# Kernel optimization log

Measured on AMD Instinct MI355X. Metric: run time of the kernel, lower is better.

## Reference

```python
import jax, jax.numpy as jnp
import numpy as np

P, D, K, E, ITERS, THRESH, NCLS = 16, 384, 16, 8, 10, 0.9, 1000


def _forward(x, pw, pb, ln_g, ln_b, pos, qw, qb, kw, kb, vw, vb,
             ew, eb, nw, nb, m1w, m1b, m2w, m2b, fbw, fbb, fgw, fgb, cw, cb):
    B, C, H, W = x.shape
    Hp, Wp = H // P, W // P
    # patch embedding: conv(k=s=P) == reshape + matmul; (c, ph, pw) ordering matches conv weight layout
    xp = x.reshape(B, C, Hp, P, Wp, P).transpose(0, 2, 4, 1, 3, 5).reshape(B, Hp * Wp, C * P * P)
    patches = xp @ pw + pb                                    # [B, N, D]
    # layer norm (eps=1e-5)
    mu = patches.mean(-1, keepdims=True)
    var = patches.var(-1, keepdims=True)
    pn = (patches - mu) / jnp.sqrt(var + 1e-5) * ln_g + ln_b
    # k-means (Lloyd, fixed iters, deterministic evenly-spaced init)
    N = pn.shape[1]
    init_idx = jnp.linspace(0, N - 1, K).astype(jnp.int32)
    centers0 = pn[:, init_idx]                                # [B, K, D]
    pn_sq = jnp.sum(pn * pn, -1)                              # [B, N]

    def kstep(centers, _):
        d2 = (pn_sq[:, :, None]
              - 2.0 * jnp.einsum('bnd,bkd->bnk', pn, centers)
              + jnp.sum(centers * centers, -1)[:, None, :])   # [B, N, K]
        oh = jax.nn.one_hot(jnp.argmin(d2, -1), K, dtype=pn.dtype)
        counts = oh.sum(1)                                    # [B, K]
        new = jnp.einsum('bnk,bnd->bkd', oh, pn) / jnp.maximum(counts, 1.0)[:, :, None]
        new = jnp.where(counts[:, :, None] > 0, new, centers)
        return new, None

    clusters, _ = jax.lax.scan(kstep, centers0, None, length=ITERS)  # [B, K, D]
    # attention over clusters
    clusters = clusters + pos
    Q = clusters @ qw + qb
    Kt = clusters @ kw + kb
    V = clusters @ vw + vb
    attn = jax.nn.softmax(jnp.einsum('bqd,bkd->bqk', Q, Kt) / jnp.sqrt(jnp.float32(D)), -1)
    clusters = jnp.einsum('bqk,bkd->bqd', attn, V)
    # hypergraph laplacian
    hw = jax.nn.softmax(clusters @ ew + eb, axis=1)           # [B, K, E], softmax over nodes
    Dd = hw.sum(1)                                            # [B, E]
    Hm = hw.transpose(0, 2, 1)                                # [B, E, K]
    M = (Dd ** -0.5)[:, :, None] * Hm                         # D^{-1/2} H
    L = jnp.eye(E, dtype=clusters.dtype) - jnp.einsum('bek,bfk->bef', M, Hm)  # [B, E, E]
    L = jnp.pad(L, ((0, 0), (0, K - E), (0, K - E)))          # pad to [B, K, K]
    clusters = jnp.einsum('bij,bjd->bid', L, clusters)
    clusters = clusters @ nw + nb
    # non-linear propagation MLP (exact GELU, torch default)
    clusters = jax.nn.gelu(clusters @ m1w + m1b, approximate=False) @ m2w + m2b
    # adaptive node collapse: mask from ORIGINAL clusters, sequential in-place merges
    nrm = jnp.maximum(jnp.linalg.norm(clusters, axis=-1, keepdims=True), 1e-12)
    nc = clusters / nrm
    sim = jnp.einsum('bqd,bkd->bqk', nc, nc)
    mask_any = jnp.any(sim > THRESH, axis=0)                  # [K, K]: merge pair if ANY batch exceeds
    for i in range(K):                                        # small fixed K; matches sequential torch loop
        for j in range(i + 1, K):
            cond = mask_any[i, j]
            merged = (clusters[:, i] + clusters[:, j]) * 0.5
            clusters = clusters.at[:, i].set(jnp.where(cond, merged, clusters[:, i]))
            clusters = clusters.at[:, j].set(jnp.where(cond, merged, clusters[:, j]))
    # feedback modulation
    g = clusters.mean(1)                                      # [B, D]
    fb = g @ fbw + fbb
    gate = jax.nn.sigmoid(g @ fgw + fgb)                      # [B, 1]
    clusters = clusters + fb[:, None, :] * gate[:, None, :]
    return clusters.reshape(B, -1) @ cw + cb                  # [B, num_classes]


def setup_inputs() -> dict:
    key = jax.random.key(0)
    ks = jax.random.split(key, 16)
    Wm = lambda k, *s: jax.random.normal(k, s, jnp.float32) * 0.02
    z = lambda *s: jnp.zeros(s, jnp.float32)
    return {
        'x': jax.random.normal(ks[0], (128, 3, 224, 224), jnp.float32),
        'pw': Wm(ks[1], 3 * P * P, D), 'pb': z(D),
        'ln_g': jnp.ones((D,), jnp.float32), 'ln_b': z(D),
        'pos': Wm(ks[2], K, D),
        'qw': Wm(ks[3], D, D), 'qb': z(D),
        'kw': Wm(ks[4], D, D), 'kb': z(D),
        'vw': Wm(ks[5], D, D), 'vb': z(D),
        'ew': Wm(ks[6], D, E), 'eb': z(E),
        'nw': Wm(ks[7], D, D), 'nb': z(D),
        'm1w': Wm(ks[8], D, D), 'm1b': z(D),
        'm2w': Wm(ks[9], D, D), 'm2b': z(D),
        'fbw': Wm(ks[10], D, D), 'fbb': z(D),
        'fgw': Wm(ks[11], D, 1), 'fgb': z(1),
        'cw': Wm(ks[12], D * K, NCLS), 'cb': z(NCLS),
    }


def reference(x, pw, pb, ln_g, ln_b, pos, qw, qb, kw, kb, vw, vb,
              ew, eb, nw, nb, m1w, m1b, m2w, m2b, fbw, fbb, fgw, fgb, cw, cb):
    return _forward(x, pw, pb, ln_g, ln_b, pos, qw, qb, kw, kb, vw, vb,
                    ew, eb, nw, nb, m1w, m1b, m2w, m2b, fbw, fbb, fgw, fgb, cw, cb)
```

## Files before the change

kernel.cpp:

```cpp
#include <hip/hip_runtime.h>
#include <math.h>

#define NBATCH 128
#define NPTS   196
#define DIN    768
#define DM     384
#define KCL    16
#define NEXP   8
#define NITER  10
#define NCLS   1000

__global__ __launch_bounds__(256) void init_kernel(const float* __restrict__ cb,
                                                   float* __restrict__ out,
                                                   int* __restrict__ mask) {
    int idx = blockIdx.x * 256 + threadIdx.x;
    if (idx < NBATCH * NCLS) {
        out[idx] = cb[idx % NCLS];
    } else if (idx < NBATCH * NCLS + 256) {
        mask[idx - NBATCH * NCLS] = 0;
    }
}

#define BKP 16
__global__ __launch_bounds__(512, 4) void patch_ln_kernel(
        const float* __restrict__ x, const float* __restrict__ pw,
        const float* __restrict__ pb, const float* __restrict__ lng,
        const float* __restrict__ lnb, float* __restrict__ pn,
        float* __restrict__ pnsq) {
    __shared__ float As[BKP * 68];
    __shared__ float Ws[BKP * DM];
    const int tid = threadIdx.x;
    const int m0  = blockIdx.x * 64;
    const int rg  = tid >> 6;
    const int cg  = tid & 63;
    const int lr = (tid & 255) >> 2, kq = tid & 3;
    const int m  = m0 + lr;
    const int bi = m / NPTS, n = m - bi * NPTS;
    const int nh = n / 14, nwp = n - nh * 14;
    const float* xb = x + (size_t)bi * 150528 + (size_t)(nh * 16) * 224 + nwp * 16;

    float acc[8][6];
#pragma unroll
    for (int r = 0; r < 8; ++r)
#pragma unroll
        for (int j = 0; j < 6; ++j) acc[r][j] = 0.f;

    const float4* pw4 = (const float4*)pw;
    for (int kc = 0; kc < DIN; kc += BKP) {
        if (tid < 256) {
            int k = kc + kq * 4;
            int c = k >> 8, py = (k >> 4) & 15, px = k & 15;
            float4 xv = *(const float4*)(xb + c * 50176 + py * 224 + px);
            As[(kq * 4 + 0) * 68 + lr] = xv.x;
            As[(kq * 4 + 1) * 68 + lr] = xv.y;
            As[(kq * 4 + 2) * 68 + lr] = xv.z;
            As[(kq * 4 + 3) * 68 + lr] = xv.w;
        }
#pragma unroll
        for (int t = 0; t < 3; ++t) {
            int s = tid + t * 512;
            ((float4*)Ws)[s] = pw4[kc * 96 + s];
        }
        __syncthreads();
#pragma unroll 4
        for (int kk = 0; kk < BKP; ++kk) {
            float a[8];
            *(float4*)&a[0] = *(const float4*)&As[kk * 68 + rg * 8];
            *(float4*)&a[4] = *(const float4*)&As[kk * 68 + rg * 8 + 4];
            float w[6];
#pragma unroll
            for (int j = 0; j < 6; ++j) w[j] = Ws[kk * DM + cg + 64 * j];
#pragma unroll
            for (int r = 0; r < 8; ++r)
#pragma unroll
                for (int j = 0; j < 6; ++j) acc[r][j] += a[r] * w[j];
        }
        __syncthreads();
    }

    float gvv[6], bvv[6], pbv[6];
#pragma unroll
    for (int j = 0; j < 6; ++j) {
        pbv[j] = pb[cg + 64 * j];
        gvv[j] = lng[cg + 64 * j];
        bvv[j] = lnb[cg + 64 * j];
    }
#pragma unroll
    for (int r = 0; r < 8; ++r) {
        float vloc[6];
        float s = 0.f;
#pragma unroll
        for (int j = 0; j < 6; ++j) { vloc[j] = acc[r][j] + pbv[j]; s += vloc[j]; }
#pragma unroll
        for (int off = 32; off >= 1; off >>= 1) s += __shfl_xor(s, off);
        float mu = s * (1.0f / DM);
        float q = 0.f;
#pragma unroll
        for (int j = 0; j < 6; ++j) { float dd = vloc[j] - mu; q += dd * dd; }
#pragma unroll
        for (int off = 32; off >= 1; off >>= 1) q += __shfl_xor(q, off);
        float rstd = rsqrtf(q * (1.0f / DM) + 1e-5f);
        float ov[6];
        float ssq = 0.f;
#pragma unroll
        for (int j = 0; j < 6; ++j) {
            float p = (vloc[j] - mu) * rstd * gvv[j] + bvv[j];
            ov[j] = p; ssq += p * p;
        }
#pragma unroll
        for (int off = 32; off >= 1; off >>= 1) ssq += __shfl_xor(ssq, off);
        int mr = m0 + rg * 8 + r;
        float* dst = pn + (size_t)mr * DM + cg;
#pragma unroll
        for (int j = 0; j < 6; ++j) dst[64 * j] = ov[j];
        if (cg == 0) pnsq[mr] = ssq;
    }
}

#define RED8(v) { v += __shfl_xor(v, 1); v += __shfl_xor(v, 2); \
                  v += __shfl_xor(v, 4); }

__global__ __launch_bounds__(1024) void kmeans_fused_kernel(
        const float* __restrict__ pn, const float* __restrict__ pnsq,
        const float* __restrict__ pos, float* __restrict__ c0) {
    __shared__ float cs[KCL * DM];
    __shared__ float cq[KCL];
    __shared__ float spq[NPTS];
    __shared__ int   asn[256];
    const int b = blockIdx.x, tid = threadIdx.x;
    const float4* pn4 = (const float4*)(pn + (size_t)b * NPTS * DM);
    float4* cs4 = (float4*)cs;

    for (int idx = tid; idx < KCL * DM / 4; idx += 1024) {
        int k = idx / 96, d4 = idx - k * 96;
        cs4[idx] = pn4[(size_t)(13 * k) * 96 + d4];
    }
    if (tid < NPTS) spq[tid] = pnsq[b * NPTS + tid];
    if (tid >= NPTS && tid < 256) asn[tid] = -1;
    __syncthreads();
    {
        const int w = tid >> 6, lane = tid & 63;
        float4 A = cs4[w * 96 + lane];
        float ss = A.x * A.x + A.y * A.y + A.z * A.z + A.w * A.w;
        if (lane < 32) {
            float4 B = cs4[w * 96 + 64 + lane];
            ss += B.x * B.x + B.y * B.y + B.z * B.z + B.w * B.w;
        }
#pragma unroll
        for (int off = 32; off >= 1; off >>= 1) ss += __shfl_xor(ss, off);
        if (lane == 0) cq[w] = ss;
    }

    const int p = tid >> 3, sub = tid & 7;
    const int p2 = p + 128;
    const bool v2 = (p2 < NPTS);
    const int p2c = v2 ? p2 : 0;
    for (int it = 0; it < NITER; ++it) {
        __syncthreads();
        float acc0[KCL], acc1[KCL];
#pragma unroll
        for (int k = 0; k < KCL; ++k) { acc0[k] = 0.f; acc1[k] = 0.f; }
#pragma unroll 2
        for (int i = 0; i < 12; ++i) {
            const int d4 = sub + 8 * i;
            float4 a0 = pn4[(size_t)p * 96 + d4];
            float4 a1 = pn4[(size_t)p2c * 96 + d4];
#pragma unroll
            for (int k = 0; k < KCL; ++k) {
                float4 c = *(const float4*)&cs[k * DM + d4 * 4];
                acc0[k] += a0.x * c.x + a0.y * c.y + a0.z * c.z + a0.w * c.w;
                acc1[k] += a1.x * c.x + a1.y * c.y + a1.z * c.z + a1.w * c.w;
            }
        }
#pragma unroll
        for (int k = 0; k < KCL; ++k) {
            float a = acc0[k]; RED8(a); acc0[k] = a;
            float d = acc1[k]; RED8(d); acc1[k] = d;
        }
        if (sub == 0) {
            {
                float mp = spq[p];
                float best = (mp - 2.0f * acc0[0]) + cq[0]; int bk = 0;
#pragma unroll
                for (int k = 1; k < KCL; ++k) {
                    float v = (mp - 2.0f * acc0[k]) + cq[k];
                    if (v < best) { best = v; bk = k; }
                }
                asn[p] = bk;
            }
            if (v2) {
                float mp = spq[p2];
                float best = (mp - 2.0f * acc1[0]) + cq[0]; int bk = 0;
#pragma unroll
                for (int k = 1; k < KCL; ++k) {
                    float v = (mp - 2.0f * acc1[k]) + cq[k];
                    if (v < best) { best = v; bk = k; }
                }
                asn[p2] = bk;
            }
        }
        __syncthreads();
        {
            const int w = tid >> 6, lane = tid & 63;
            float4 sA = make_float4(0.f, 0.f, 0.f, 0.f);
            float4 sB = make_float4(0.f, 0.f, 0.f, 0.f);
            int c = 0;
#pragma unroll
            for (int ch = 0; ch < 4; ++ch) {
                int a = asn[ch * 64 + lane];
                unsigned long long m = __ballot(a == w);
                c += __popcll(m);
                while (m) {
                    int nn = ch * 64 + (int)__builtin_ctzll(m);
                    m &= m - 1;
                    float4 vA = pn4[(size_t)nn * 96 + lane];
                    sA.x += vA.x; sA.y += vA.y; sA.z += vA.z; sA.w += vA.w;
                    if (lane < 32) {
                        float4 vB = pn4[(size_t)nn * 96 + 64 + lane];
                        sB.x += vB.x; sB.y += vB.y; sB.z += vB.z; sB.w += vB.w;
                    }
                }
            }
            float4 nA, nB = make_float4(0.f, 0.f, 0.f, 0.f);
            if (c > 0) {
                float inv = 1.0f / (float)c;
                nA.x = sA.x * inv; nA.y = sA.y * inv; nA.z = sA.z * inv; nA.w = sA.w * inv;
                if (lane < 32) {
                    nB.x = sB.x * inv; nB.y = sB.y * inv; nB.z = sB.z * inv; nB.w = sB.w * inv;
                }
            } else {
                nA = cs4[w * 96 + lane];
                if (lane < 32) nB = cs4[w * 96 + 64 + lane];
            }
            cs4[w * 96 + lane] = nA;
            if (lane < 32) cs4[w * 96 + 64 + lane] = nB;
            float ss = nA.x * nA.x + nA.y * nA.y + nA.z * nA.z + nA.w * nA.w
                     + nB.x * nB.x + nB.y * nB.y + nB.z * nB.z + nB.w * nB.w;
#pragma unroll
            for (int off = 32; off >= 1; off >>= 1) ss += __shfl_xor(ss, off);
            if (lane == 0) cq[w] = ss;
        }
    }
    __syncthreads();
    const float4* pos4 = (const float4*)pos;
    float4* c0b = (float4*)(c0 + (size_t)b * KCL * DM);
    for (int idx = tid; idx < KCL * DM / 4; idx += 1024) {
        float4 cv = cs4[idx];
        float4 pv = pos4[idx];
        cv.x += pv.x; cv.y += pv.y; cv.z += pv.z; cv.w += pv.w;
        c0b[idx] = cv;
    }
}

__global__ __launch_bounds__(256) void gemm_qkv_kernel(
        const float* __restrict__ A,
        const float* __restrict__ qw, const float* __restrict__ kw,
        const float* __restrict__ vw,
        const float* __restrict__ qb, const float* __restrict__ kb,
        const float* __restrict__ vb,
        float* __restrict__ Q, float* __restrict__ K, float* __restrict__ V) {
    __shared__ float As[32 * 32];
    __shared__ float Ws[3][32 * 128];
    const int n0 = blockIdx.x * 128;
    const int m0 = blockIdx.y * 32;
    const int tid = threadIdx.x;
    const int rg = tid >> 5, cg = tid & 31;
    const int arow = tid >> 3, akg = tid & 7;
    const float* W[3] = {qw, kw, vw};

    float acc[3][4][4];
#pragma unroll
    for (int g = 0; g < 3; ++g)
#pragma unroll
        for (int r = 0; r < 4; ++r)
#pragma unroll
            for (int j = 0; j < 4; ++j) acc[g][r][j] = 0.f;

    for (int kc = 0; kc < DM; kc += 32) {
        float4 av = *(const float4*)(A + (size_t)(m0 + arow) * DM + kc + akg * 4);
        As[(akg * 4 + 0) * 32 + arow] = av.x;
        As[(akg * 4 + 1) * 32 + arow] = av.y;
        As[(akg * 4 + 2) * 32 + arow] = av.z;
        As[(akg * 4 + 3) * 32 + arow] = av.w;
#pragma unroll
        for (int g = 0; g < 3; ++g)
#pragma unroll
            for (int t = 0; t < 4; ++t) {
                int s = tid + t * 256;
                int kk = s >> 5, c4i = s & 31;
                *(float4*)&Ws[g][kk * 128 + c4i * 4] =
                    *(const float4*)(W[g] + (size_t)(kc + kk) * DM + n0 + c4i * 4);
            }
        __syncthreads();
#pragma unroll 8
        for (int kk = 0; kk < 32; ++kk) {
            float4 a = *(const float4*)&As[kk * 32 + rg * 4];
            float ar[4] = {a.x, a.y, a.z, a.w};
#pragma unroll
            for (int g = 0; g < 3; ++g) {
                float4 w = *(const float4*)&Ws[g][kk * 128 + cg * 4];
                float wr[4] = {w.x, w.y, w.z, w.w};
#pragma unroll
                for (int r = 0; r < 4; ++r)
#pragma unroll
                    for (int j = 0; j < 4; ++j) acc[g][r][j] += ar[r] * wr[j];
            }
        }
        __syncthreads();
    }
    const float* B[3] = {qb, kb, vb};
    float* O[3] = {Q, K, V};
#pragma unroll
    for (int g = 0; g < 3; ++g) {
        float4 bv = *(const float4*)(B[g] + n0 + cg * 4);
        float bvr[4] = {bv.x, bv.y, bv.z, bv.w};
#pragma unroll
        for (int r = 0; r < 4; ++r) {
            float o[4];
#pragma unroll
            for (int j = 0; j < 4; ++j) o[j] = acc[g][r][j] + bvr[j];
            *(float4*)(O[g] + (size_t)(m0 + rg * 4 + r) * DM + n0 + cg * 4) =
                *(float4*)&o[0];
        }
    }
}

template <int ACT>
__global__ __launch_bounds__(256) void gemm_kernel(
        const float* __restrict__ A, const float* __restrict__ W,
        const float* __restrict__ bias, float* __restrict__ out,
        int M, int N, int Kd) {
    __shared__ float As[32 * 32];
    __shared__ float Ws[32 * 128];
    const int n0 = blockIdx.x * 128;
    const int m0 = blockIdx.y * 32;
    const int tid = threadIdx.x;
    const int rg = tid >> 5, cg = tid & 31;
    const int arow = tid >> 3, akg = tid & 7;
    float acc[4][4];
#pragma unroll
    for (int r = 0; r < 4; ++r)
#pragma unroll
        for (int j = 0; j < 4; ++j) acc[r][j] = 0.f;

    for (int kc = 0; kc < Kd; kc += 32) {
        float4 av = *(const float4*)(A + (size_t)(m0 + arow) * Kd + kc + akg * 4);
        As[(akg * 4 + 0) * 32 + arow] = av.x;
        As[(akg * 4 + 1) * 32 + arow] = av.y;
        As[(akg * 4 + 2) * 32 + arow] = av.z;
        As[(akg * 4 + 3) * 32 + arow] = av.w;
#pragma unroll
        for (int t = 0; t < 4; ++t) {
            int s = tid + t * 256;
            int kk = s >> 5, c4i = s & 31;
            *(float4*)&Ws[kk * 128 + c4i * 4] =
                *(const float4*)(W + (size_t)(kc + kk) * N + n0 + c4i * 4);
        }
        __syncthreads();
#pragma unroll 16
        for (int kk = 0; kk < 32; ++kk) {
            float4 a = *(const float4*)&As[kk * 32 + rg * 4];
            float4 w = *(const float4*)&Ws[kk * 128 + cg * 4];
            float ar[4] = {a.x, a.y, a.z, a.w};
            float wr[4] = {w.x, w.y, w.z, w.w};
#pragma unroll
            for (int r = 0; r < 4; ++r)
#pragma unroll
                for (int j = 0; j < 4; ++j) acc[r][j] += ar[r] * wr[j];
        }
        __syncthreads();
    }
    float4 bv = *(const float4*)(bias + n0 + cg * 4);
    float bvr[4] = {bv.x, bv.y, bv.z, bv.w};
#pragma unroll
    for (int r = 0; r < 4; ++r) {
        float o[4];
#pragma unroll
        for (int j = 0; j < 4; ++j) {
            float v = acc[r][j] + bvr[j];
            if (ACT == 1) v = 0.5f * v * (1.0f + erff(v * 0.70710678118654752440f));
            o[j] = v;
        }
        *(float4*)(out + (size_t)(m0 + rg * 4 + r) * N + n0 + cg * 4) = *(float4*)&o[0];
    }
}

__global__ __launch_bounds__(256) void attn_spectral_kernel(
        const float* __restrict__ Qg, const float* __restrict__ Kg,
        const float* __restrict__ Vg, const float* __restrict__ ew,
        const float* __restrict__ eb, float* __restrict__ c2) {
    __shared__ float Qs[KCL * 388];
    __shared__ float Ks[KCL * 388];
    __shared__ float ewt[NEXP * 388];
    __shared__ float Ss[KCL * 17];
    __shared__ float hws[KCL * 9];
    __shared__ float rds[NEXP];
    __shared__ float Ls[NEXP * NEXP];
    const int b = blockIdx.x, tid = threadIdx.x;
    for (int idx = tid; idx < KCL * DM; idx += 256) {
        int i = idx / DM, d = idx - i * DM;
        size_t g = (size_t)b * KCL * DM + idx;
        Qs[i * 388 + d] = Qg[g];
        Ks[i * 388 + d] = Kg[g];
    }
    for (int idx = tid; idx < DM * NEXP; idx += 256) {
        int d = idx >> 3, e = idx & 7;
        ewt[e * 388 + d] = ew[idx];
    }
    __syncthreads();
    {
        int i = tid >> 4, j = tid & 15;
        float acc = 0.f;
        for (int d = 0; d < DM; d += 4) {
            float4 q = *(const float4*)&Qs[i * 388 + d];
            float4 k = *(const float4*)&Ks[j * 388 + d];
            acc += q.x * k.x + q.y * k.y + q.z * k.z + q.w * k.w;
        }
        float s = acc / sqrtf((float)DM);
        float mx = s;
#pragma unroll
        for (int off = 8; off >= 1; off >>= 1) mx = fmaxf(mx, __shfl_xor(mx, off));
        float p = expf(s - mx);
        float sm = p;
#pragma unroll
        for (int off = 8; off >= 1; off >>= 1) sm += __shfl_xor(sm, off);
        Ss[i * 17 + j] = p / sm;
    }
    __syncthreads();
    for (int idx = tid; idx < KCL * DM; idx += 256) {
        int i = idx / DM, d = idx - i * DM;
        Ks[i * 388 + d] = Vg[(size_t)b * KCL * DM + idx];
    }
    __syncthreads();
    for (int idx = tid; idx < KCL * DM; idx += 256) {
        int i = idx / DM, d = idx - i * DM;
        float acc = 0.f;
#pragma unroll
        for (int j = 0; j < KCL; ++j) acc += Ss[i * 17 + j] * Ks[j * 388 + d];
        Qs[i * 388 + d] = acc;
    }
    __syncthreads();
    if (tid < 128) {
        int e = tid >> 4, i = tid & 15;
        float l = 0.f;
        for (int d4 = 0; d4 < DM / 4; ++d4) {
            float4 q = *(const float4*)&Qs[i * 388 + d4 * 4];
            float4 w = *(const float4*)&ewt[e * 388 + d4 * 4];
            l += q.x * w.x + q.y * w.y + q.z * w.z + q.w * w.w;
        }
        l += eb[e];
        float mx = l;
#pragma unroll
        for (int off = 8; off >= 1; off >>= 1) mx = fmaxf(mx, __shfl_xor(mx, off));
        float p = expf(l - mx);
        float sm = p;
#pragma unroll
        for (int off = 8; off >= 1; off >>= 1) sm += __shfl_xor(sm, off);
        float h = p / sm;
        hws[i * 9 + e] = h;
        float sd = h;
#pragma unroll
        for (int off = 8; off >= 1; off >>= 1) sd += __shfl_xor(sd, off);
        if (i == 0) rds[e] = 1.0f / sqrtf(sd);
    }
    __syncthreads();
    if (tid < 64) {
        int e = tid >> 3, f = tid & 7;
        float gsum = 0.f;
#pragma unroll
        for (int k = 0; k < KCL; ++k) gsum += hws[k * 9 + e] * hws[k * 9 + f];
        Ls[e * 8 + f] = ((e == f) ? 1.0f : 0.0f) - rds[e] * gsum;
    }
    __syncthreads();
    for (int idx = tid; idx < KCL * DM; idx += 256) {
        int i = idx / DM, d = idx - i * DM;
        float acc = 0.f;
        if (i < NEXP) {
#pragma unroll
            for (int j = 0; j < NEXP; ++j) acc += Ls[i * 8 + j] * Qs[j * 388 + d];
        }
        c2[(size_t)b * KCL * DM + idx] = acc;
    }
}

__global__ __launch_bounds__(256) void simmask_kernel(const float* __restrict__ c4,
                                                      int* __restrict__ mask) {
    __shared__ float Cs[KCL * 388];
    __shared__ float rns[KCL];
    const int b = blockIdx.x, tid = threadIdx.x;
    for (int idx = tid; idx < KCL * DM; idx += 256) {
        int i = idx / DM, d = idx - i * DM;
        Cs[i * 388 + d] = c4[(size_t)b * KCL * DM + idx];
    }
    __syncthreads();
    {
        int i = tid >> 4, s = tid & 15;
        float ss = 0.f;
        for (int t = 0; t < 24; ++t) { float v = Cs[i * 388 + s + 16 * t]; ss += v * v; }
#pragma unroll
        for (int off = 8; off >= 1; off >>= 1) ss += __shfl_xor(ss, off);
        if (s == 0) rns[i] = 1.0f / fmaxf(sqrtf(ss), 1e-12f);
    }
    __syncthreads();
    for (int idx = tid; idx < KCL * DM; idx += 256) {
        int i = idx / DM, d = idx - i * DM;
        Cs[i * 388 + d] *= rns[i];
    }
    __syncthreads();
    {
        int i = tid >> 4, j = tid & 15;
        if (j > i) {
            float dp = 0.f;
            for (int d = 0; d < DM; d += 4) {
                float4 a = *(const float4*)&Cs[i * 388 + d];
                float4 c = *(const float4*)&Cs[j * 388 + d];
                dp += a.x * c.x + a.y * c.y + a.z * c.z + a.w * c.w;
            }
            if (dp > 0.9f) atomicOr(&mask[i * KCL + j], 1);
        }
    }
}

__global__ __launch_bounds__(256) void merge_fb_kernel(
        const float* __restrict__ c4, const int* __restrict__ mask,
        const float* __restrict__ fbw, const float* __restrict__ fbb,
        const float* __restrict__ fgw, const float* __restrict__ fgb,
        float* __restrict__ c5) {
    __shared__ int   mk[256];
    __shared__ float gs[DM];
    __shared__ float wred[3];
    __shared__ float gatev;
    const int b = blockIdx.x, tid = threadIdx.x;
    mk[tid] = mask[tid];
    const bool act = tid < 192;
    const int t = tid;
    float2 v[KCL];
    if (act) {
#pragma unroll
        for (int i = 0; i < KCL; ++i)
            v[i] = *(const float2*)(c4 + (size_t)b * KCL * DM + i * DM + 2 * t);
    }
    __syncthreads();
    if (act) {
#pragma unroll
        for (int i = 0; i < KCL; ++i)
#pragma unroll
            for (int j = i + 1; j < KCL; ++j)
                if (mk[i * KCL + j]) {
                    float mx = 0.5f * (v[i].x + v[j].x);
                    float my = 0.5f * (v[i].y + v[j].y);
                    v[i].x = mx; v[i].y = my; v[j].x = mx; v[j].y = my;
                }
    }
    float2 gv = {0.f, 0.f};
    if (act) {
#pragma unroll
        for (int i = 0; i < KCL; ++i) { gv.x += v[i].x; gv.y += v[i].y; }
        gv.x *= 0.0625f; gv.y *= 0.0625f;
        gs[2 * t] = gv.x; gs[2 * t + 1] = gv.y;
    }
    float pg = act ? (gv.x * fgw[2 * t] + gv.y * fgw[2 * t + 1]) : 0.f;
#pragma unroll
    for (int off = 32; off >= 1; off >>= 1) pg += __shfl_xor(pg, off);
    if (act && (tid & 63) == 0) wred[tid >> 6] = pg;
    __syncthreads();
    if (tid == 0) {
        float d = wred[0] + wred[1] + wred[2] + fgb[0];
        gatev = 1.0f / (1.0f + expf(-d));
    }
    __syncthreads();
    if (act) {
        float fx = fbb[2 * t], fy = fbb[2 * t + 1];
        for (int j = 0; j < DM; ++j) {
            float gj = gs[j];
            const float2 w = *(const float2*)(fbw + (size_t)j * DM + 2 * t);
            fx += gj * w.x; fy += gj * w.y;
        }
        float gt = gatev;
#pragma unroll
        for (int i = 0; i < KCL; ++i) {
            float2 o = {v[i].x + fx * gt, v[i].y + fy * gt};
            *(float2*)(c5 + (size_t)b * KCL * DM + i * DM + 2 * t) = o;
        }
    }
}

__global__ __launch_bounds__(256) void cls_kernel(const float* __restrict__ A,
                                                  const float* __restrict__ Wt,
                                                  float* __restrict__ out) {
    __shared__ float As[32 * 32];
    __shared__ float Ws[32 * 128];
    const int n0 = blockIdx.x * 128;
    const int m0 = blockIdx.y * 32;
    const int k0 = blockIdx.z * 768;
    const int tid = threadIdx.x;
    const int rg = tid >> 5, cg = tid & 31;
    const int arow = tid >> 3, akg = tid & 7;
    float acc[4][4];
#pragma unroll
    for (int r = 0; r < 4; ++r)
#pragma unroll
        for (int j = 0; j < 4; ++j) acc[r][j] = 0.f;

    for (int kc = k0; kc < k0 + 768; kc += 32) {
        float4 av = *(const float4*)(A + (size_t)(m0 + arow) * (KCL * DM) + kc + akg * 4);
        As[(akg * 4 + 0) * 32 + arow] = av.x;
        As[(akg * 4 + 1) * 32 + arow] = av.y;
        As[(akg * 4 + 2) * 32 + arow] = av.z;
        As[(akg * 4 + 3) * 32 + arow] = av.w;
#pragma unroll
        for (int ti = 0; ti < 4; ++ti) {
            int s = tid + ti * 256;
            int kk = s >> 5, c4i = s & 31;
            int col = n0 + c4i * 4;
            float4 wv = make_float4(0.f, 0.f, 0.f, 0.f);
            if (col < NCLS) wv = *(const float4*)(Wt + (size_t)(kc + kk) * NCLS + col);
            *(float4*)&Ws[kk * 128 + c4i * 4] = wv;
        }
        __syncthreads();
#pragma unroll 16
        for (int kk = 0; kk < 32; ++kk) {
            float4 a = *(const float4*)&As[kk * 32 + rg * 4];
            float4 w = *(const float4*)&Ws[kk * 128 + cg * 4];
            float ar[4] = {a.x, a.y, a.z, a.w};
            float wr[4] = {w.x, w.y, w.z, w.w};
#pragma unroll
            for (int r = 0; r < 4; ++r)
#pragma unroll
                for (int j = 0; j < 4; ++j) acc[r][j] += ar[r] * wr[j];
        }
        __syncthreads();
    }
    int col = n0 + cg * 4;
    if (col < NCLS) {
#pragma unroll
        for (int r = 0; r < 4; ++r) {
            int row = m0 + rg * 4 + r;
#pragma unroll
            for (int j = 0; j < 4; ++j)
                atomicAdd(&out[(size_t)row * NCLS + col + j], acc[r][j]);
        }
    }
}

extern "C" void kernel_launch(void* const* d_in, const int* in_sizes, int n_in,
                              void* d_out, int out_size, void* d_ws, size_t ws_size,
                              hipStream_t stream) {
    const float* x   = (const float*)d_in[0];
    const float* pw  = (const float*)d_in[1];
    const float* pb  = (const float*)d_in[2];
    const float* lng = (const float*)d_in[3];
    const float* lnb = (const float*)d_in[4];
    const float* pos = (const float*)d_in[5];
    const float* qw  = (const float*)d_in[6];
    const float* qb  = (const float*)d_in[7];
    const float* kw  = (const float*)d_in[8];
    const float* kb  = (const float*)d_in[9];
    const float* vw  = (const float*)d_in[10];
    const float* vb  = (const float*)d_in[11];
    const float* ew  = (const float*)d_in[12];
    const float* eb  = (const float*)d_in[13];
    const float* nw  = (const float*)d_in[14];
    const float* nb  = (const float*)d_in[15];
    const float* m1w = (const float*)d_in[16];
    const float* m1b = (const float*)d_in[17];
    const float* m2w = (const float*)d_in[18];
    const float* m2b = (const float*)d_in[19];
    const float* fbw = (const float*)d_in[20];
    const float* fbb = (const float*)d_in[21];
    const float* fgw = (const float*)d_in[22];
    const float* fgb = (const float*)d_in[23];
    const float* cw  = (const float*)d_in[24];
    const float* cb  = (const float*)d_in[25];
    float* out = (float*)d_out;
    float* ws  = (float*)d_ws;

    float* pn_   = ws;
    float* pnsq_ = ws + 9633792;
    float* c0_   = ws + 9658880;
    float* Q_    = ws + 10445312;
    float* K_    = ws + 11231744;
    float* V_    = ws + 12018176;
    float* c2_   = ws + 12804608;
    int*   mask_ = (int*)(ws + 13591040);
    float* c3_ = Q_;
    float* h_  = K_;
    float* c4_ = V_;
    float* c5_ = c0_;

    init_kernel<<<501, 256, 0, stream>>>(cb, out, mask_);
    patch_ln_kernel<<<392, 512, 0, stream>>>(x, pw, pb, lng, lnb, pn_, pnsq_);

    kmeans_fused_kernel<<<NBATCH, 1024, 0, stream>>>(pn_, pnsq_, pos, c0_);

    gemm_qkv_kernel<<<dim3(3, 64), 256, 0, stream>>>(c0_, qw, kw, vw, qb, kb, vb,
                                                     Q_, K_, V_);
    attn_spectral_kernel<<<NBATCH, 256, 0, stream>>>(Q_, K_, V_, ew, eb, c2_);
    gemm_kernel<0><<<dim3(3, 64), 256, 0, stream>>>(c2_, nw, nb, c3_, 2048, DM, DM);
    gemm_kernel<1><<<dim3(3, 64), 256, 0, stream>>>(c3_, m1w, m1b, h_, 2048, DM, DM);
    gemm_kernel<0><<<dim3(3, 64), 256, 0, stream>>>(h_, m2w, m2b, c4_, 2048, DM, DM);
    simmask_kernel<<<NBATCH, 256, 0, stream>>>(c4_, mask_);
    merge_fb_kernel<<<NBATCH, 256, 0, stream>>>(c4_, mask_, fbw, fbb, fgw, fgb, c5_);
    cls_kernel<<<dim3(8, 4, 8), 256, 0, stream>>>(c5_, cw, out);
}
```

Baseline: 965.5 us.

## Register-prefetch patch GEMM tiles and k-means loads; batch centroid gathers via member lists

The patch-embedding GEMM now loads the next K-chunk of inputs and weights into registers while computing the current chunk, so global latency overlaps the FMA loop. The k-means distance loop prefetches point vectors two steps ahead. Centroid updates first compact each cluster's member indices into a shared list, then gather four rows at a time to expose more memory parallelism than the serial ballot loop. These add register pressure and about 12.8KB of shared memory in the k-means kernel, which is already near its limits.

```diff
diff --git a/kernel.cpp b/kernel.cpp
--- a/kernel.cpp
+++ b/kernel.cpp
@@ -46,22 +46,39 @@
         for (int j = 0; j < 6; ++j) acc[r][j] = 0.f;
 
     const float4* pw4 = (const float4*)pw;
+    float4 xv = make_float4(0.f, 0.f, 0.f, 0.f);
+    float4 wv0, wv1, wv2;
+    if (tid < 256) {
+        int k = kq * 4;
+        int c = k >> 8, py = (k >> 4) & 15, px = k & 15;
+        xv = *(const float4*)(xb + c * 50176 + py * 224 + px);
+    }
+    wv0 = pw4[tid];
+    wv1 = pw4[tid + 512];
+    wv2 = pw4[tid + 1024];
+
     for (int kc = 0; kc < DIN; kc += BKP) {
         if (tid < 256) {
-            int k = kc + kq * 4;
-            int c = k >> 8, py = (k >> 4) & 15, px = k & 15;
-            float4 xv = *(const float4*)(xb + c * 50176 + py * 224 + px);
             As[(kq * 4 + 0) * 68 + lr] = xv.x;
             As[(kq * 4 + 1) * 68 + lr] = xv.y;
             As[(kq * 4 + 2) * 68 + lr] = xv.z;
             As[(kq * 4 + 3) * 68 + lr] = xv.w;
         }
-#pragma unroll
-        for (int t = 0; t < 3; ++t) {
-            int s = tid + t * 512;
-            ((float4*)Ws)[s] = pw4[kc * 96 + s];
-        }
-        __syncthreads();
+        ((float4*)Ws)[tid]        = wv0;
+        ((float4*)Ws)[tid + 512]  = wv1;
+        ((float4*)Ws)[tid + 1024] = wv2;
+        __syncthreads();
+        const int kn = kc + BKP;
+        if (kn < DIN) {
+            if (tid < 256) {
+                int k = kn + kq * 4;
+                int c = k >> 8, py = (k >> 4) & 15, px = k & 15;
+                xv = *(const float4*)(xb + c * 50176 + py * 224 + px);
+            }
+            wv0 = pw4[kn * 96 + tid];
+            wv1 = pw4[kn * 96 + tid + 512];
+            wv2 = pw4[kn * 96 + tid + 1024];
+        }
 #pragma unroll 4
         for (int kk = 0; kk < BKP; ++kk) {
             float a[8];
@@ -127,6 +144,7 @@
     __shared__ float cq[KCL];
     __shared__ float spq[NPTS];
     __shared__ int   asn[256];
+    __shared__ int   lst[KCL * 200];
     const int b = blockIdx.x, tid = threadIdx.x;
     const float4* pn4 = (const float4*)(pn + (size_t)b * NPTS * DM);
     float4* cs4 = (float4*)cs;
@@ -160,17 +178,25 @@
         float acc0[KCL], acc1[KCL];
 #pragma unroll
         for (int k = 0; k < KCL; ++k) { acc0[k] = 0.f; acc1[k] = 0.f; }
-#pragma unroll 2
+        float4 a0c = pn4[(size_t)p * 96 + sub];
+        float4 a1c = pn4[(size_t)p2c * 96 + sub];
+        float4 a0n = pn4[(size_t)p * 96 + sub + 8];
+        float4 a1n = pn4[(size_t)p2c * 96 + sub + 8];
+#pragma unroll
         for (int i = 0; i < 12; ++i) {
+            float4 a0f = a0c, a1f = a1c;
+            if (i + 2 < 12) {
+                a0f = pn4[(size_t)p * 96 + sub + 8 * (i + 2)];
+                a1f = pn4[(size_t)p2c * 96 + sub + 8 * (i + 2)];
+            }
             const int d4 = sub + 8 * i;
-            float4 a0 = pn4[(size_t)p * 96 + d4];
-            float4 a1 = pn4[(size_t)p2c * 96 + d4];
 #pragma unroll
             for (int k = 0; k < KCL; ++k) {
                 float4 c = *(const float4*)&cs[k * DM + d4 * 4];
-                acc0[k] += a0.x * c.x + a0.y * c.y + a0.z * c.z + a0.w * c.w;
-                acc1[k] += a1.x * c.x + a1.y * c.y + a1.z * c.z + a1.w * c.w;
-            }
+                acc0[k] += a0c.x * c.x + a0c.y * c.y + a0c.z * c.z + a0c.w * c.w;
+                acc1[k] += a1c.x * c.x + a1c.y * c.y + a1c.z * c.z + a1c.w * c.w;
+            }
+            a0c = a0n; a1c = a1n; a0n = a0f; a1n = a1f;
         }
 #pragma unroll
         for (int k = 0; k < KCL; ++k) {
@@ -202,28 +228,59 @@
         __syncthreads();
         {
             const int w = tid >> 6, lane = tid & 63;
+            int cnt = 0;
+#pragma unroll
+            for (int ch = 0; ch < 4; ++ch) {
+                int a = asn[ch * 64 + lane];
+                unsigned long long mm = __ballot(a == w);
+                if (a == w) {
+                    int r = __popcll(mm & ((1ull << lane) - 1ull));
+                    lst[w * 200 + cnt + r] = ch * 64 + lane;
+                }
+                cnt += __popcll(mm);
+            }
             float4 sA = make_float4(0.f, 0.f, 0.f, 0.f);
             float4 sB = make_float4(0.f, 0.f, 0.f, 0.f);
-            int c = 0;
-#pragma unroll
-            for (int ch = 0; ch < 4; ++ch) {
-                int a = asn[ch * 64 + lane];
-                unsigned long long m = __ballot(a == w);
-                c += __popcll(m);
-                while (m) {
-                    int nn = ch * 64 + (int)__builtin_ctzll(m);
-                    m &= m - 1;
-                    float4 vA = pn4[(size_t)nn * 96 + lane];
-                    sA.x += vA.x; sA.y += vA.y; sA.z += vA.z; sA.w += vA.w;
-                    if (lane < 32) {
-                        float4 vB = pn4[(size_t)nn * 96 + 64 + lane];
-                        sB.x += vB.x; sB.y += vB.y; sB.z += vB.z; sB.w += vB.w;
-                    }
+            int i = 0;
+            for (; i + 4 <= cnt; i += 4) {
+                int n0 = lst[w * 200 + i];
+                int n1 = lst[w * 200 + i + 1];
+                int n2 = lst[w * 200 + i + 2];
+                int n3 = lst[w * 200 + i + 3];
+                float4 vA0 = pn4[(size_t)n0 * 96 + lane];
+                float4 vA1 = pn4[(size_t)n1 * 96 + lane];
+                float4 vA2 = pn4[(size_t)n2 * 96 + lane];
+                float4 vA3 = pn4[(size_t)n3 * 96 + lane];
+                float4 vB0, vB1, vB2, vB3;
+                if (lane < 32) {
+                    vB0 = pn4[(size_t)n0 * 96 + 64 + lane];
+                    vB1 = pn4[(size_t)n1 * 96 + 64 + lane];
+                    vB2 = pn4[(size_t)n2 * 96 + 64 + lane];
+                    vB3 = pn4[(size_t)n3 * 96 + 64 + lane];
                 }
+                sA.x += vA0.x; sA.y += vA0.y; sA.z += vA0.z; sA.w += vA0.w;
+                sA.x += vA1.x; sA.y += vA1.y; sA.z += vA1.z; sA.w += vA1.w;
+                sA.x += vA2.x; sA.y += vA2.y; sA.z += vA2.z; sA.w += vA2.w;
+                sA.x += vA3.x; sA.y += vA3.y; sA.z += vA3.z; sA.w += vA3.w;
+                if (lane < 32) {
+                    sB.x += vB0.x; sB.y += vB0.y; sB.z += vB0.z; sB.w += vB0.w;
+                    sB.x += vB1.x; sB.y += vB1.y; sB.z += vB1.z; sB.w += vB1.w;
+                    sB.x += vB2.x; sB.y += vB2.y; sB.z += vB2.z; sB.w += vB2.w;
+                    sB.x += vB3.x; sB.y += vB3.y; sB.z += vB3.z; sB.w += vB3.w;
+                }
+            }
+            for (; i < cnt; ++i) {
+                int nn = lst[w * 200 + i];
+                float4 vA = pn4[(size_t)nn * 96 + lane];
+                sA.x += vA.x; sA.y += vA.y; sA.z += vA.z; sA.w += vA.w;
+                if (lane < 32) {
+                    float4 vB = pn4[(size_t)nn * 96 + 64 + lane];
+                    sB.x += vB.x; sB.y += vB.y; sB.z += vB.z; sB.w += vB.w;
+                }
             }
             float4 nA, nB = make_float4(0.f, 0.f, 0.f, 0.f);
-            if (c > 0) {
-                float inv = 1.0f / (float)c;
+            if (cnt > 0) {
+                float inv = 1.0f / (float)cnt;
                 nA.x = sA.x * inv; nA.y = sA.y * inv; nA.z = sA.z * inv; nA.w = sA.w * inv;
                 if (lane < 32) {
                     nB.x = sB.x * inv; nB.y = sB.y * inv; nB.z = sB.z * inv; nB.w = sB.w * inv;
```

New measurement: 1.313 ms. +36.0%, slower.
